# Optimization experiments

Measured on AMD Instinct MI355X. Metric: run time of the kernel, lower is better.

## Reference

```python
import jax, jax.numpy as jnp
import numpy as np

N, E, IN, H1, H2, A, B, MAXB = 57344, 458752, 128, 256, 64, 11, 16, 4096
GD = H1  # g_dim = hidden1


def _lin(k, i, o):
    return jax.random.normal(k, (i, o), jnp.float32) / np.sqrt(i).astype(np.float32)


def setup_inputs():
    key = jax.random.key(0)
    ks = jax.random.split(key, 24)
    x = jax.random.normal(ks[0], (N, IN), jnp.float32)
    x = x.at[:, 0].set(1.0)  # every node is a host (x[:,0]==1)
    ei = jax.random.randint(ks[1], (2, E), 0, N, dtype=jnp.int32)
    sizes = [4096] * 12 + [2048] * 4  # sums to N
    batches = jnp.asarray(np.concatenate([[0], np.cumsum(sizes)]), jnp.int32)
    inp = {
        'x': x, 'ei': ei, 'batches': batches, 'max_batch': MAXB,
        'conv1_w': _lin(ks[2], IN, H1), 'conv1_b': jnp.zeros((H1,), jnp.float32),
        'conv2_w': _lin(ks[3], H1, H2), 'conv2_b': jnp.zeros((H2,), jnp.float32),
        # SimpleSelfAttention g0: in=IN, h=H1, g=GD
        'g0_aw': _lin(ks[4], IN, H1), 'g0_ab': jnp.zeros((H1,), jnp.float32),
        'g0_fw': _lin(ks[5], IN, H1), 'g0_fb': jnp.zeros((H1,), jnp.float32),
        'g0_gw': _lin(ks[6], H1 + GD, GD), 'g0_gb': jnp.zeros((GD,), jnp.float32),
        # g1: in=H1, h=H1, g=GD
        'g1_aw': _lin(ks[7], H1, H1), 'g1_ab': jnp.zeros((H1,), jnp.float32),
        'g1_fw': _lin(ks[8], H1, H1), 'g1_fb': jnp.zeros((H1,), jnp.float32),
        'g1_gw': _lin(ks[9], H1 + GD, GD), 'g1_gb': jnp.zeros((GD,), jnp.float32),
        # g2: in=H2, h=H2, g=GD
        'g2_aw': _lin(ks[10], H2, H2), 'g2_ab': jnp.zeros((H2,), jnp.float32),
        'g2_fw': _lin(ks[11], H2, H2), 'g2_fb': jnp.zeros((H2,), jnp.float32),
        'g2_gw': _lin(ks[12], H2 + GD, GD), 'g2_gb': jnp.zeros((GD,), jnp.float32),
        # out MLP head
        'o1_w': _lin(ks[13], H2 + GD, H1), 'o1_b': jnp.zeros((H1,), jnp.float32),
        'o2_w': _lin(ks[14], H1, A), 'o2_b': jnp.zeros((A,), jnp.float32),
    }
    return inp


def reference(x, ei, batches, max_batch,
              conv1_w, conv1_b, conv2_w, conv2_b,
              g0_aw, g0_ab, g0_fw, g0_fb, g0_gw, g0_gb,
              g1_aw, g1_ab, g1_fw, g1_fb, g1_gw, g1_gb,
              g2_aw, g2_ab, g2_fw, g2_fb, g2_gw, g2_gb,
              o1_w, o1_b, o2_w, o2_b):
    n = x.shape[0]
    nb = batches.shape[0] - 1
    idx = jnp.arange(n, dtype=jnp.int32)
    # all nodes are hosts; CSR -> (batch_id, position) for vectorized pad_and_pack
    batch_id = jnp.searchsorted(batches, idx, side='right').astype(jnp.int32) - 1
    pos = idx - batches[batch_id]
    mask = jnp.zeros((nb, max_batch, 1), x.dtype).at[batch_id, pos].set(1.0)

    def pack(h):  # [n, d] -> [nb, max_batch, d] with zero padding
        return jnp.zeros((nb, max_batch, h.shape[-1]), h.dtype).at[batch_id, pos].set(h)

    src_sl = jnp.concatenate([ei[0], idx])  # add self loops
    dst_sl = jnp.concatenate([ei[1], idx])

    def gcn(h, W, b):  # GCNConv: D^{-1/2}(A+I)D^{-1/2} h W + b (deg from target col)
        deg = jax.ops.segment_sum(jnp.ones_like(dst_sl, h.dtype), dst_sl, num_segments=n)
        dis = jnp.where(deg > 0, jax.lax.rsqrt(jnp.maximum(deg, 1.0)), 0.0)
        norm = dis[src_sl] * dis[dst_sl]
        hw = h @ W
        return jax.ops.segment_sum(hw[src_sl] * norm[:, None], dst_sl, num_segments=n) + b

    def attn(v, g, aw, ab, fw, fb, gw, gb):  # SimpleSelfAttention
        att = jax.nn.softmax(v @ aw + ab, axis=-1) * mask
        feat = v @ fw + fb
        o = jnp.sum(att * feat, axis=1)  # [nb, h]
        return g + (jnp.concatenate([o, g], axis=-1) @ gw + gb)

    g = attn(pack(x), jnp.zeros((nb, GD), x.dtype), g0_aw, g0_ab, g0_fw, g0_fb, g0_gw, g0_gb)
    h = jax.nn.relu(gcn(x, conv1_w, conv1_b))
    g = attn(pack(h), g, g1_aw, g1_ab, g1_fw, g1_fb, g1_gw, g1_gb)
    h = jax.nn.relu(gcn(h, conv2_w, conv2_b))
    g = attn(pack(h), g, g2_aw, g2_ab, g2_fw, g2_fb, g2_gw, g2_gb)

    host_z = jnp.concatenate([h, g[batch_id]], axis=1)  # repeat_interleave via gather
    actions = jax.nn.relu(host_z @ o1_w + o1_b) @ o2_w + o2_b  # [n, A]
    out = pack(actions)  # [nb, max_batch, A]
    out = jnp.where(mask > 0, out, -jnp.inf)
    return out.reshape(nb, max_batch * A)  # Categorical logits
```

## Files before the change

kernel.cpp:

```cpp
#include <hip/hip_runtime.h>
#include <math.h>

#define N_NODES 57344
#define N_EDGES 458752
#define DIM_IN 128
#define DIM_H1 256
#define DIM_H2 64
#define DIM_A 11
#define NB 16
#define MAXB 4096
#define OUT_PER_B (MAXB*DIM_A)
#define OUT_SZ (NB*OUT_PER_B)
#define NEG_FILL (-1.0e30f)

typedef unsigned short u16;
typedef unsigned int u32;
typedef __bf16 bf16x8 __attribute__((ext_vector_type(8)));
typedef float f32x4 __attribute__((ext_vector_type(4)));

__device__ __forceinline__ float bflo(u32 u){ union{u32 i; float f;} x; x.i = u<<16; return x.f; }
__device__ __forceinline__ float bfhi(u32 u){ union{u32 i; float f;} x; x.i = u & 0xFFFF0000u; return x.f; }
__device__ __forceinline__ u32 f2bf(float f){ union{float f; u32 i;} x; x.f=f; return (x.i + 0x7FFFu + ((x.i>>16)&1u)) >> 16; }

__device__ __forceinline__ float wave_max(float v){
  #pragma unroll
  for (int off=32; off; off>>=1) v = fmaxf(v, __shfl_xor(v, off));
  return v;
}
__device__ __forceinline__ float wave_sum(float v){
  #pragma unroll
  for (int off=32; off; off>>=1) v += __shfl_xor(v, off);
  return v;
}

__global__ __launch_bounds__(256) void k_init(int* cnt, int* bid, const int* __restrict__ batches,
                                              float* oacc, float* out){
  int i = blockIdx.x*256 + threadIdx.x;
  if (i < N_NODES){
    cnt[i] = 0;
    int lo=0, hi=NB-1;
    while (lo<hi){ int mid=(lo+hi+1)>>1; if (batches[mid]<=i) lo=mid; else hi=mid-1; }
    bid[i]=lo;
  }
  if (i < 3*NB*256) oacc[i] = 0.0f;
  if (i < OUT_SZ) out[i] = NEG_FILL;
}

__global__ __launch_bounds__(256) void k_deg(const int* __restrict__ ei, int* cnt){
  int e = blockIdx.x*256 + threadIdx.x;
  if (e < N_EDGES) atomicAdd(&cnt[ei[N_EDGES + e]], 1);
}

__global__ __launch_bounds__(256) void k_scanA(const int* __restrict__ cnt, int* bsum){
  __shared__ int s[256];
  int t=threadIdx.x; int i=blockIdx.x*256+t;
  s[t]=cnt[i]; __syncthreads();
  for (int off=128; off; off>>=1){ if (t<off) s[t]+=s[t+off]; __syncthreads(); }
  if (t==0) bsum[blockIdx.x]=s[0];
}
__global__ __launch_bounds__(256) void k_scanB(const int* __restrict__ bsum, int* boff){
  __shared__ int s[256];
  int t=threadIdx.x;
  int v = (t < N_NODES/256) ? bsum[t] : 0;
  s[t]=v; __syncthreads();
  for (int o=1;o<256;o<<=1){
    int a = (t>=o) ? s[t-o] : 0;
    __syncthreads();
    s[t] += a;
    __syncthreads();
  }
  if (t < N_NODES/256) boff[t] = s[t] - v;
}
__global__ __launch_bounds__(256) void k_scanC(const int* __restrict__ cnt, const int* __restrict__ boff,
                                               int* rowstart, int* cursor, float* dis){
  __shared__ int s[256];
  int t=threadIdx.x; int i=blockIdx.x*256+t;
  int v=cnt[i]; s[t]=v; __syncthreads();
  for (int off=1; off<256; off<<=1){
    int add = (t>=off)? s[t-off] : 0;
    __syncthreads();
    s[t]+=add;
    __syncthreads();
  }
  int rs = boff[blockIdx.x] + s[t] - v;
  rowstart[i]=rs; cursor[i]=rs;
  dis[i] = rsqrtf(1.0f + (float)v);
}
__global__ __launch_bounds__(256) void k_place(const int* __restrict__ ei, int* cursor, int* csr_src){
  int e = blockIdx.x*256 + threadIdx.x;
  if (e < N_EDGES){
    int s = ei[e], d = ei[N_EDGES+e];
    int slot = atomicAdd(&cursor[d], 1);
    csr_src[slot] = s;
  }
}

__global__ __launch_bounds__(256) void k_cvtx(const float* __restrict__ x, u16* __restrict__ xb){
  int i = blockIdx.x*256 + threadIdx.x;
  float4 v = *(const float4*)(x + (size_t)i*4);
  u32 lo = f2bf(v.x) | (f2bf(v.y)<<16);
  u32 hi = f2bf(v.z) | (f2bf(v.w)<<16);
  *(uint2*)(xb + (size_t)i*4) = make_uint2(lo, hi);
}

__global__ __launch_bounds__(256) void k_prep(
    const float* __restrict__ conv1_w, const float* __restrict__ g0_aw, const float* __restrict__ g0_fw,
    const float* __restrict__ g1_aw, const float* __restrict__ g1_fw, const float* __restrict__ conv2_w,
    const float* __restrict__ g2_aw, const float* __restrict__ g2_fw, const float* __restrict__ o1_w,
    const float* __restrict__ g0_ab, const float* __restrict__ g0_fb,
    const float* __restrict__ g1_ab, const float* __restrict__ g1_fb,
    const float* __restrict__ g2_ab, const float* __restrict__ g2_fb,
    u16* conv1T, u16* Wt0, u16* Wt1, u16* conv2T, u16* Wt2, u16* o1T,
    float* cb0, float* cb1, float* cb2){
  int i = blockIdx.x*256 + threadIdx.x;
  if (i < 32768){ int k=i>>8, n=i&255; conv1T[n*128+k]=(u16)f2bf(conv1_w[i]); return; } i-=32768;
  if (i < 32768){ int k=i>>8, n=i&255; Wt0[n*128+k]=(u16)f2bf(g0_aw[i]); return; } i-=32768;
  if (i < 32768){ int k=i>>8, n=i&255; Wt0[(256+n)*128+k]=(u16)f2bf(g0_fw[i]); return; } i-=32768;
  if (i < 65536){ int k=i>>8, n=i&255; Wt1[n*256+k]=(u16)f2bf(g1_aw[i]); return; } i-=65536;
  if (i < 65536){ int k=i>>8, n=i&255; Wt1[(256+n)*256+k]=(u16)f2bf(g1_fw[i]); return; } i-=65536;
  if (i < 16384){ int k=i>>6, n=i&63;  conv2T[n*256+k]=(u16)f2bf(conv2_w[i]); return; } i-=16384;
  if (i < 4096) { int k=i>>6, n=i&63;  Wt2[n*64+k]=(u16)f2bf(g2_aw[i]); return; } i-=4096;
  if (i < 4096) { int k=i>>6, n=i&63;  Wt2[(64+n)*64+k]=(u16)f2bf(g2_fw[i]); return; } i-=4096;
  if (i < 16384){ int k=i>>8, n=i&255; o1T[n*64+k]=(u16)f2bf(o1_w[i]); return; } i-=16384;
  if (i < 256){ cb0[i]=g0_ab[i]; return; } i-=256;
  if (i < 256){ cb0[256+i]=g0_fb[i]; return; } i-=256;
  if (i < 256){ cb1[i]=g1_ab[i]; return; } i-=256;
  if (i < 256){ cb1[256+i]=g1_fb[i]; return; } i-=256;
  if (i < 64) { cb2[i]=g2_ab[i]; return; } i-=64;
  if (i < 64) { cb2[64+i]=g2_fb[i]; return; }
}

__global__ __launch_bounds__(256) void k_agg1b(const u16* __restrict__ xb, const float* __restrict__ dis,
        const int* __restrict__ rowstart, const int* __restrict__ cnt, const int* __restrict__ csr_src,
        u16* __restrict__ agg){
  int d = (blockIdx.x*256 + threadIdx.x) >> 6;
  int lane = threadIdx.x & 63;
  float dd = dis[d];
  u32 u = *(const u32*)(xb + (size_t)d*DIM_IN + lane*2);
  float ax = bflo(u)*dd*dd, ay = bfhi(u)*dd*dd;
  int base = rowstart[d], c = cnt[d];
  int j = 0;
  for (; j+4 <= c; j += 4){
    int s0=csr_src[base+j+0], s1=csr_src[base+j+1], s2=csr_src[base+j+2], s3=csr_src[base+j+3];
    u32 u0=*(const u32*)(xb+(size_t)s0*DIM_IN+lane*2);
    u32 u1=*(const u32*)(xb+(size_t)s1*DIM_IN+lane*2);
    u32 u2=*(const u32*)(xb+(size_t)s2*DIM_IN+lane*2);
    u32 u3=*(const u32*)(xb+(size_t)s3*DIM_IN+lane*2);
    float n0=dis[s0]*dd, n1=dis[s1]*dd, n2=dis[s2]*dd, n3=dis[s3]*dd;
    ax=fmaf(bflo(u0),n0,ax); ay=fmaf(bfhi(u0),n0,ay);
    ax=fmaf(bflo(u1),n1,ax); ay=fmaf(bfhi(u1),n1,ay);
    ax=fmaf(bflo(u2),n2,ax); ay=fmaf(bfhi(u2),n2,ay);
    ax=fmaf(bflo(u3),n3,ax); ay=fmaf(bfhi(u3),n3,ay);
  }
  for (; j<c; ++j){
    int s = csr_src[base+j];
    float nrm = dis[s]*dd;
    u32 us = *(const u32*)(xb + (size_t)s*DIM_IN + lane*2);
    ax = fmaf(bflo(us), nrm, ax);
    ay = fmaf(bfhi(us), nrm, ay);
  }
  *(u32*)(agg + (size_t)d*DIM_IN + lane*2) = f2bf(ax) | (f2bf(ay)<<16);
}

__global__ __launch_bounds__(256) void k_agg2b(const u16* __restrict__ hw, const float* __restrict__ dis,
        const int* __restrict__ rowstart, const int* __restrict__ cnt, const int* __restrict__ csr_src,
        const float* __restrict__ b2, u16* __restrict__ h2){
  int d = (blockIdx.x*256 + threadIdx.x) >> 6;
  int lane = threadIdx.x & 63;
  float dd = dis[d];
  float acc = bflo((u32)hw[(size_t)d*DIM_H2 + lane]) * dd*dd;
  int base = rowstart[d], c = cnt[d];
  int j = 0;
  for (; j+4 <= c; j += 4){
    int s0=csr_src[base+j+0], s1=csr_src[base+j+1], s2=csr_src[base+j+2], s3=csr_src[base+j+3];
    u16 v0=hw[(size_t)s0*DIM_H2+lane], v1=hw[(size_t)s1*DIM_H2+lane];
    u16 v2=hw[(size_t)s2*DIM_H2+lane], v3=hw[(size_t)s3*DIM_H2+lane];
    float n0=dis[s0]*dd, n1=dis[s1]*dd, n2=dis[s2]*dd, n3=dis[s3]*dd;
    acc=fmaf(bflo((u32)v0),n0,acc); acc=fmaf(bflo((u32)v1),n1,acc);
    acc=fmaf(bflo((u32)v2),n2,acc); acc=fmaf(bflo((u32)v3),n3,acc);
  }
  for (; j<c; ++j){
    int s = csr_src[base+j];
    acc = fmaf(bflo((u32)hw[(size_t)s*DIM_H2 + lane]), dis[s]*dd, acc);
  }
  h2[(size_t)d*DIM_H2 + lane] = (u16)f2bf(fmaxf(acc + b2[lane], 0.0f));
}

__global__ __launch_bounds__(256) void k_mm(const u16* __restrict__ A, const u16* __restrict__ Wt,
        const float* __restrict__ bias, const float* __restrict__ rowbias, const int* __restrict__ bid,
        u16* __restrict__ C, int K, int Ncol, int flags){
  __shared__ u16 As[128][40];
  __shared__ u16 Bs[64][40];
  const int t = threadIdx.x;
  const int row0 = blockIdx.x*128, col0 = blockIdx.y*64;
  const int lane = t & 63, w = t >> 6;
  const int lr = lane & 15, q = lane >> 4;
  f32x4 acc[2][4];
  #pragma unroll
  for (int r=0;r<2;++r){
    #pragma unroll
    for (int c=0;c<4;++c){ f32x4 z = {}; acc[r][c] = z; }
  }
  for (int k0=0; k0<K; k0+=32){
    #pragma unroll
    for (int i=0;i<2;++i){
      int ch = t + i*256;
      int r = ch>>2, ko = (ch&3)*8;
      *(uint4*)(&As[r][ko]) = *(const uint4*)(A + (size_t)(row0+r)*K + k0 + ko);
    }
    {
      int r = t>>2, ko = (t&3)*8;
      *(uint4*)(&Bs[r][ko]) = *(const uint4*)(Wt + (size_t)(col0+r)*K + k0 + ko);
    }
    __syncthreads();
    bf16x8 af0 = *(const bf16x8*)(&As[w*32 + lr][q*8]);
    bf16x8 af1 = *(const bf16x8*)(&As[w*32 + 16 + lr][q*8]);
    #pragma unroll
    for (int c=0;c<4;++c){
      bf16x8 bfr = *(const bf16x8*)(&Bs[c*16 + lr][q*8]);
      acc[0][c] = __builtin_amdgcn_mfma_f32_16x16x32_bf16(af0, bfr, acc[0][c], 0,0,0);
      acc[1][c] = __builtin_amdgcn_mfma_f32_16x16x32_bf16(af1, bfr, acc[1][c], 0,0,0);
    }
    __syncthreads();
  }
  float bcol[4];
  #pragma unroll
  for (int c=0;c<4;++c){
    int col = col0 + c*16 + lr;
    float bv = 0.f;
    if (flags & 4) bv += bias[col];
    if (flags & 2) bv += rowbias[(size_t)bid[row0]*Ncol + col];
    bcol[c] = bv;
  }
  #pragma unroll
  for (int r=0;r<2;++r){
    #pragma unroll
    for (int c=0;c<4;++c){
      int col = col0 + c*16 + lr;
      #pragma unroll
      for (int i=0;i<4;++i){
        int row = row0 + w*32 + r*16 + q*4 + i;
        float v = acc[r][c][i] + bcol[c];
        if (flags & 1) v = fmaxf(v, 0.f);
        C[(size_t)row*Ncol + col] = (u16)f2bf(v);
      }
    }
  }
}

template<int DIN, int H>
__global__ __launch_bounds__(256) void k_attnf(const u16* __restrict__ V, const u16* __restrict__ Wt,
        const float* __restrict__ cb, const int* __restrict__ bid, float* __restrict__ o){
  constexpr int CF  = H/64;
  constexpr int KS  = DIN/32;
  constexpr int AST = DIN + 8;
  constexpr int SST = H + 4;
  __shared__ u16 As[32*AST];
  __shared__ u16 Ssh[32*SST];
  __shared__ u16 Fsh[32*SST];
  __shared__ float mZ[2][32];
  const int t = threadIdx.x;
  const int node0 = blockIdx.x*32;
  const int lane = t & 63, w = t >> 6;
  const int lr = lane & 15, q = lane >> 4;
  #pragma unroll
  for (int i = 0; i < (32*DIN/8)/256; ++i){
    int ch = t + i*256;
    int r = ch / (DIN/8), co = (ch % (DIN/8))*8;
    *(uint4*)(&As[r*AST + co]) = *(const uint4*)(V + (size_t)(node0+r)*DIN + co);
  }
  __syncthreads();
  #pragma unroll
  for (int ph = 0; ph < 2; ++ph){
    f32x4 acc[2][CF];
    #pragma unroll
    for (int r=0;r<2;++r){
      #pragma unroll
      for (int c=0;c<CF;++c){ f32x4 z = {}; acc[r][c] = z; }
    }
    #pragma unroll
    for (int k=0;k<KS;++k){
      bf16x8 a0 = *(const bf16x8*)(&As[lr*AST + k*32 + q*8]);
      bf16x8 a1 = *(const bf16x8*)(&As[(16+lr)*AST + k*32 + q*8]);
      #pragma unroll
      for (int c=0;c<CF;++c){
        int col = ph*H + w*(16*CF) + c*16 + lr;
        bf16x8 b = *(const bf16x8*)(Wt + (size_t)col*DIN + k*32 + q*8);
        acc[0][c] = __builtin_amdgcn_mfma_f32_16x16x32_bf16(a0, b, acc[0][c], 0,0,0);
        acc[1][c] = __builtin_amdgcn_mfma_f32_16x16x32_bf16(a1, b, acc[1][c], 0,0,0);
      }
    }
    u16* dst = ph ? Fsh : Ssh;
    #pragma unroll
    for (int c=0;c<CF;++c){
      int colL = w*(16*CF) + c*16 + lr;
      float bias = cb[ph*H + colL];
      #pragma unroll
      for (int rf=0; rf<2; ++rf){
        #pragma unroll
        for (int i=0;i<4;++i){
          int row = rf*16 + q*4 + i;
          dst[row*SST + colL] = (u16)f2bf(acc[rf][c][i] + bias);
        }
      }
    }
    if (ph==0){
      __syncthreads();
      #pragma unroll
      for (int nn=0; nn<8; ++nn){
        int n = w*8 + nn;
        constexpr int VPL = H/64;
        float vals[VPL]; float mx = -1e30f;
        if constexpr (VPL == 4){
          uint2 uv = *(const uint2*)(&Ssh[n*SST + lane*4]);
          vals[0]=bflo(uv.x); vals[1]=bfhi(uv.x); vals[2]=bflo(uv.y); vals[3]=bfhi(uv.y);
          mx = fmaxf(fmaxf(vals[0],vals[1]), fmaxf(vals[2],vals[3]));
        } else {
          vals[0] = bflo((u32)Ssh[n*SST + lane]);
          mx = vals[0];
        }
        mx = wave_max(mx);
        float z = 0.f;
        #pragma unroll
        for (int i=0;i<VPL;++i) z += __expf(vals[i]-mx);
        z = wave_sum(z);
        if (lane==0){ mZ[0][n]=mx; mZ[1][n]=1.0f/z; }
      }
    }
  }
  __syncthreads();
  const int col = t % H;
  constexpr int NPER = 32*H/256;
  const int n0 = (t / H) * NPER;
  float acc2 = 0.f;
  #pragma unroll 8
  for (int n=n0; n<n0+NPER; ++n){
    float s = bflo((u32)Ssh[n*SST + col]);
    float f = bflo((u32)Fsh[n*SST + col]);
    acc2 = fmaf(__expf(s - mZ[0][n]) * mZ[1][n], f, acc2);
  }
  atomicAdd(&o[bid[node0]*H + col], acc2);
}

template<int H, bool HASG>
__global__ __launch_bounds__(256) void k_gup2(const float* __restrict__ o, const float* __restrict__ gprev,
        const float* __restrict__ gw, const float* __restrict__ gb, float* __restrict__ gout){
  constexpr int KT = H + (HASG ? 256 : 0);
  constexpr int KPS = KT/8;
  __shared__ float vsh[KT];
  __shared__ float red[8][33];
  const int b = blockIdx.x;
  const int c = threadIdx.x & 31;
  const int s = threadIdx.x >> 5;
  const int col = blockIdx.y*32 + c;
  for (int k=threadIdx.x; k<KT; k+=256)
    vsh[k] = (k < H) ? o[b*H + k] : gprev[b*256 + (k - H)];
  __syncthreads();
  float acc = 0.f;
  const float* wp = gw + (size_t)(s*KPS)*256 + col;
  #pragma unroll 8
  for (int i=0;i<KPS;++i)
    acc = fmaf(vsh[s*KPS+i], wp[(size_t)i*256], acc);
  red[s][c] = acc;
  __syncthreads();
  if (s==0){
    float sum = 0.f;
    #pragma unroll
    for (int j=0;j<8;++j) sum += red[j][c];
    float gp = HASG ? gprev[b*256+col] : 0.f;
    gout[b*256+col] = gp + sum + gb[col];
  }
}

__global__ __launch_bounds__(256) void k_hb2(const float* __restrict__ g2, const float* __restrict__ o1w,
                                             const float* __restrict__ o1b, float* __restrict__ hb){
  __shared__ float vsh[256];
  __shared__ float red[8][33];
  const int b = blockIdx.x;
  const int c = threadIdx.x & 31;
  const int s = threadIdx.x >> 5;
  const int col = blockIdx.y*32 + c;
  vsh[threadIdx.x] = g2[b*256 + threadIdx.x];
  __syncthreads();
  float acc = 0.f;
  const float* wp = o1w + (size_t)(64 + s*32)*256 + col;
  #pragma unroll 8
  for (int i=0;i<32;++i)
    acc = fmaf(vsh[s*32+i], wp[(size_t)i*256], acc);
  red[s][c] = acc;
  __syncthreads();
  if (s==0){
    float sum = 0.f;
    #pragma unroll
    for (int j=0;j<8;++j) sum += red[j][c];
    hb[b*256+col] = sum + o1b[col];
  }
}

__global__ __launch_bounds__(256) void k_head2(const u16* __restrict__ z, const float* __restrict__ w,
        const float* __restrict__ bvec, const int* __restrict__ bid, const int* __restrict__ batches,
        float* __restrict__ out){
  __shared__ float zs[16][257];
  int t = threadIdx.x;
  int g0 = blockIdx.x*16;
  #pragma unroll
  for (int i=0;i<2;++i){
    int ch = t + i*256;
    int v = ch>>5, ko=(ch&31)*8;
    uint4 qv = *(const uint4*)(z + (size_t)(g0+v)*256 + ko);
    zs[v][ko+0]=bflo(qv.x); zs[v][ko+1]=bfhi(qv.x);
    zs[v][ko+2]=bflo(qv.y); zs[v][ko+3]=bfhi(qv.y);
    zs[v][ko+4]=bflo(qv.z); zs[v][ko+5]=bfhi(qv.z);
    zs[v][ko+6]=bflo(qv.w); zs[v][ko+7]=bfhi(qv.w);
  }
  __syncthreads();
  int v = t >> 4, c = t & 15;
  if (c < DIM_A){
    float acc = bvec[c];
    for (int k=0;k<256;++k) acc = fmaf(zs[v][k], w[k*DIM_A + c], acc);
    int node = g0 + v;
    int bb = bid[node];
    out[(size_t)bb*OUT_PER_B + (size_t)(node - batches[bb])*DIM_A + c] = acc;
  }
}

extern "C" void kernel_launch(void* const* d_in, const int* in_sizes, int n_in,
                              void* d_out, int out_size, void* d_ws, size_t ws_size,
                              hipStream_t stream){
  const float* x       = (const float*)d_in[0];
  const int*   ei      = (const int*)d_in[1];
  const int*   batches = (const int*)d_in[2];
  const float* conv1_w = (const float*)d_in[4];
  const float* conv1_b = (const float*)d_in[5];
  const float* conv2_w = (const float*)d_in[6];
  const float* conv2_b = (const float*)d_in[7];
  const float* g0_aw = (const float*)d_in[8];  const float* g0_ab = (const float*)d_in[9];
  const float* g0_fw = (const float*)d_in[10]; const float* g0_fb = (const float*)d_in[11];
  const float* g0_gw = (const float*)d_in[12]; const float* g0_gb = (const float*)d_in[13];
  const float* g1_aw = (const float*)d_in[14]; const float* g1_ab = (const float*)d_in[15];
  const float* g1_fw = (const float*)d_in[16]; const float* g1_fb = (const float*)d_in[17];
  const float* g1_gw = (const float*)d_in[18]; const float* g1_gb = (const float*)d_in[19];
  const float* g2_aw = (const float*)d_in[20]; const float* g2_ab = (const float*)d_in[21];
  const float* g2_fw = (const float*)d_in[22]; const float* g2_fb = (const float*)d_in[23];
  const float* g2_gw = (const float*)d_in[24]; const float* g2_gb = (const float*)d_in[25];
  const float* o1_w  = (const float*)d_in[26]; const float* o1_b  = (const float*)d_in[27];
  const float* o2_w  = (const float*)d_in[28]; const float* o2_b  = (const float*)d_in[29];
  float* out = (float*)d_out;

  char* W = (char*)d_ws;
  size_t off = 0;
  auto alloc = [&](size_t bytes)->void*{
    off = (off + 255) & ~(size_t)255;
    void* p = W + off; off += bytes; return p;
  };
  float* dis      = (float*)alloc(N_NODES*4);
  int*   cnt      = (int*)  alloc(N_NODES*4);
  int*   bid      = (int*)  alloc(N_NODES*4);
  int*   rowstart = (int*)  alloc(N_NODES*4);
  int*   cursor   = (int*)  alloc(N_NODES*4);
  int*   csr_src  = (int*)  alloc(N_EDGES*4);
  int*   bsum     = (int*)  alloc(256*4);
  int*   boff     = (int*)  alloc(256*4);
  float* o0       = (float*)alloc(NB*256*4);
  float* o1a      = (float*)alloc(NB*256*4);
  float* o2a      = (float*)alloc(NB*256*4);
  float* gv0      = (float*)alloc(NB*256*4);
  float* gv1      = (float*)alloc(NB*256*4);
  float* gv2      = (float*)alloc(NB*256*4);
  float* hb       = (float*)alloc(NB*256*4);
  float* cb0      = (float*)alloc(512*4);
  float* cb1      = (float*)alloc(512*4);
  float* cb2      = (float*)alloc(128*4);
  u16* conv1T = (u16*)alloc(32768*2);
  u16* Wt0    = (u16*)alloc(65536*2);
  u16* Wt1    = (u16*)alloc(131072*2);
  u16* conv2T = (u16*)alloc(16384*2);
  u16* Wt2    = (u16*)alloc(8192*2);
  u16* o1T    = (u16*)alloc(16384*2);
  u16* h1b    = (u16*)alloc((size_t)N_NODES*DIM_H1*2);
  u16* X      = (u16*)alloc((size_t)N_NODES*DIM_IN*2);
  u16* agg1b  = (u16*)alloc((size_t)N_NODES*DIM_IN*2);
  u16* xb    = X;
  u16* hw2b  = X;
  u16* h2b   = X + (size_t)N_NODES*DIM_H2;
  u16* z     = h1b;

  k_init <<<OUT_SZ/256, 256, 0, stream>>>(cnt, bid, batches, o0, out);
  k_deg  <<<N_EDGES/256, 256, 0, stream>>>(ei, cnt);
  k_scanA<<<N_NODES/256, 256, 0, stream>>>(cnt, bsum);
  k_scanB<<<1, 256, 0, stream>>>(bsum, boff);
  k_scanC<<<N_NODES/256, 256, 0, stream>>>(cnt, boff, rowstart, cursor, dis);
  k_place<<<N_EDGES/256, 256, 0, stream>>>(ei, cursor, csr_src);

  k_cvtx <<<N_NODES*DIM_IN/4/256, 256, 0, stream>>>(x, xb);
  k_prep <<<(270336+1152+255)/256, 256, 0, stream>>>(conv1_w, g0_aw, g0_fw, g1_aw, g1_fw, conv2_w,
            g2_aw, g2_fw, o1_w, g0_ab, g0_fb, g1_ab, g1_fb, g2_ab, g2_fb,
            conv1T, Wt0, Wt1, conv2T, Wt2, o1T, cb0, cb1, cb2);

  k_agg1b<<<N_NODES/4, 256, 0, stream>>>(xb, dis, rowstart, cnt, csr_src, agg1b);
  k_mm   <<<dim3(N_NODES/128, 4), 256, 0, stream>>>(agg1b, conv1T, conv1_b, nullptr, nullptr,
                                                    h1b, DIM_IN, DIM_H1, 4|1);
  k_attnf<128,256><<<N_NODES/32, 256, 0, stream>>>(xb, Wt0, cb0, bid, o0);
  k_gup2<256,false><<<dim3(NB,8), 256, 0, stream>>>(o0, nullptr, g0_gw, g0_gb, gv0);

  k_attnf<256,256><<<N_NODES/32, 256, 0, stream>>>(h1b, Wt1, cb1, bid, o1a);
  k_gup2<256,true><<<dim3(NB,8), 256, 0, stream>>>(o1a, gv0, g1_gw, g1_gb, gv1);

  k_mm   <<<dim3(N_NODES/128, 1), 256, 0, stream>>>(h1b, conv2T, nullptr, nullptr, nullptr,
                                                    hw2b, DIM_H1, DIM_H2, 0);
  k_agg2b<<<N_NODES/4, 256, 0, stream>>>(hw2b, dis, rowstart, cnt, csr_src, conv2_b, h2b);

  k_attnf<64,64><<<N_NODES/32, 256, 0, stream>>>(h2b, Wt2, cb2, bid, o2a);
  k_gup2<64,true><<<dim3(NB,8), 256, 0, stream>>>(o2a, gv1, g2_gw, g2_gb, gv2);

  k_hb2  <<<dim3(NB,8), 256, 0, stream>>>(gv2, o1_w, o1_b, hb);
  k_mm   <<<dim3(N_NODES/128, 4), 256, 0, stream>>>(h2b, o1T, nullptr, hb, bid, z, DIM_H2, 256, 2|1);
  k_head2<<<N_NODES/16, 256, 0, stream>>>(z, o2_w, o2_b, bid, batches, out);

  (void)in_sizes; (void)n_in; (void)out_size; (void)ws_size;
}
```

Baseline: 469.5 us.

## Rewrite attention kernel to keep softmax rows and features in registers

```diff
diff --git a/kernel.cpp b/kernel.cpp
--- a/kernel.cpp
+++ b/kernel.cpp
@@ -244,6 +244,93 @@
         if (flags & 1) v = fmaxf(v, 0.f);
         C[(size_t)row*Ncol + col] = (u16)f2bf(v);
       }
+    }
+  }
+}
+
+template<int DIN>
+__global__ __launch_bounds__(256) void k_attnf2(const u16* __restrict__ V, const u16* __restrict__ Wt,
+        const float* __restrict__ cb, const int* __restrict__ bid, float* __restrict__ o){
+  constexpr int H = 256;
+  constexpr int KS = DIN/32;
+  constexpr int AST = DIN + 8;
+  constexpr int PST = H + 8;
+  __shared__ u16 As[32*AST];
+  __shared__ u16 Psh[32*PST];
+  const int t = threadIdx.x;
+  const int node0 = blockIdx.x*32;
+  const int lane = t & 63, w = t >> 6;
+  const int lr = lane & 15, q = lane >> 4;
+  const bool isS = (w < 2);
+  const int rw = w & 1;
+  #pragma unroll
+  for (int i = 0; i < (32*DIN/8)/256; ++i){
+    int ch = t + i*256;
+    int r = ch / (DIN/8), co = (ch % (DIN/8))*8;
+    *(uint4*)(&As[r*AST + co]) = *(const uint4*)(V + (size_t)(node0+r)*DIN + co);
+  }
+  __syncthreads();
+  f32x4 acc[16];
+  #pragma unroll
+  for (int c=0;c<16;++c){ f32x4 z = {}; acc[c] = z; }
+  const u16* Wbase = Wt + (size_t)(isS ? 0 : H)*DIN;
+  #pragma unroll
+  for (int k=0;k<KS;++k){
+    bf16x8 a = *(const bf16x8*)(&As[(rw*16 + lr)*AST + k*32 + q*8]);
+    #pragma unroll
+    for (int c=0;c<16;++c){
+      bf16x8 b = *(const bf16x8*)(Wbase + (size_t)(c*16 + lr)*DIN + k*32 + q*8);
+      acc[c] = __builtin_amdgcn_mfma_f32_16x16x32_bf16(a, b, acc[c], 0,0,0);
+    }
+  }
+  #pragma unroll
+  for (int c=0;c<16;++c){
+    float bv = cb[(isS ? 0 : H) + c*16 + lr];
+    #pragma unroll
+    for (int i=0;i<4;++i) acc[c][i] += bv;
+  }
+  if (isS){
+    float m[4], iz[4];
+    #pragma unroll
+    for (int i=0;i<4;++i){
+      float mx = acc[0][i];
+      #pragma unroll
+      for (int c=1;c<16;++c) mx = fmaxf(mx, acc[c][i]);
+      #pragma unroll
+      for (int off=1; off<16; off<<=1) mx = fmaxf(mx, __shfl_xor(mx, off));
+      m[i] = mx;
+    }
+    #pragma unroll
+    for (int i=0;i<4;++i){
+      float s = 0.f;
+      #pragma unroll
+      for (int c=0;c<16;++c) s += __expf(acc[c][i] - m[i]);
+      #pragma unroll
+      for (int off=1; off<16; off<<=1) s += __shfl_xor(s, off);
+      iz[i] = 1.0f/s;
+    }
+    #pragma unroll
+    for (int c=0;c<16;++c){
+      #pragma unroll
+      for (int i=0;i<4;++i){
+        Psh[(rw*16 + q*4 + i)*PST + c*16 + lr] = (u16)f2bf(__expf(acc[c][i]-m[i])*iz[i]);
+      }
+    }
+  }
+  __syncthreads();
+  if (!isS){
+    const int b = bid[node0];
+    #pragma unroll
+    for (int c=0;c<16;++c){
+      float cs = 0.f;
+      #pragma unroll
+      for (int i=0;i<4;++i){
+        float p = bflo((u32)Psh[(rw*16 + q*4 + i)*PST + c*16 + lr]);
+        cs = fmaf(p, acc[c][i], cs);
+      }
+      cs += __shfl_xor(cs, 16);
+      cs += __shfl_xor(cs, 32);
+      if (q == (c & 3)) atomicAdd(&o[b*H + c*16 + lr], cs);
     }
   }
 }
@@ -500,10 +587,10 @@
   k_agg1b<<<N_NODES/4, 256, 0, stream>>>(xb, dis, rowstart, cnt, csr_src, agg1b);
   k_mm   <<<dim3(N_NODES/128, 4), 256, 0, stream>>>(agg1b, conv1T, conv1_b, nullptr, nullptr,
                                                     h1b, DIM_IN, DIM_H1, 4|1);
-  k_attnf<128,256><<<N_NODES/32, 256, 0, stream>>>(xb, Wt0, cb0, bid, o0);
+  k_attnf2<128><<<N_NODES/32, 256, 0, stream>>>(xb, Wt0, cb0, bid, o0);
   k_gup2<256,false><<<dim3(NB,8), 256, 0, stream>>>(o0, nullptr, g0_gw, g0_gb, gv0);
 
-  k_attnf<256,256><<<N_NODES/32, 256, 0, stream>>>(h1b, Wt1, cb1, bid, o1a);
+  k_attnf2<256><<<N_NODES/32, 256, 0, stream>>>(h1b, Wt1, cb1, bid, o1a);
   k_gup2<256,true><<<dim3(NB,8), 256, 0, stream>>>(o1a, gv0, g1_gw, g1_gb, gv1);
 
   k_mm   <<<dim3(N_NODES/128, 1), 256, 0, stream>>>(h1b, conv2T, nullptr, nullptr, nullptr,
```

Measured after the change: 539.5 us. 1.15x slower.
